# Kernel tuning notes

Hardware: AMD Instinct MI355X
Metric: run time of the kernel (lower is better)

Reference implementation:

```python
import jax, jax.numpy as jnp
import numpy as np

L, B, H, E, V = 64, 2048, 512, 50, 96
PAD = 0  # padding_idx of the char embedding


def setup_inputs() -> dict:
    key = jax.random.key(0)
    ks = jax.random.split(key, 10)
    s = 0.1  # param scale to keep gates in a sane range
    emb = jax.random.normal(ks[0], (V, E), jnp.float32) * s
    emb = emb.at[PAD].set(0.0)  # padding_idx row is zero
    return {
        "input_ids": jax.random.randint(ks[1], (L, B), 0, V),
        "h0": jax.random.normal(ks[2], (1, B, H), jnp.float32) * s,
        "c0": jax.random.normal(ks[3], (1, B, H), jnp.float32) * s,
        "emb": emb,
        "W_ih": jax.random.normal(ks[4], (4 * H, E), jnp.float32) * s,
        "W_hh": jax.random.normal(ks[5], (4 * H, H), jnp.float32) * s,
        "b_ih": jax.random.normal(ks[6], (4 * H,), jnp.float32) * s,
        "b_hh": jax.random.normal(ks[7], (4 * H,), jnp.float32) * s,
        "W_out": jax.random.normal(ks[8], (V, H), jnp.float32) * s,
        "b_out": jax.random.normal(ks[9], (V,), jnp.float32) * s,
    }


def reference(input_ids, h0, c0, emb, W_ih, W_hh, b_ih, b_hh, W_out, b_out):
    # Embedding lookup: (L, B, E)
    x = emb[input_ids]
    # Precompute input-side gate contributions for all steps: (L, B, 4H)
    x_gates = jnp.einsum('lbe,ge->lbg', x, W_ih) + b_ih + b_hh

    def step(carry, xg):
        h, c = carry  # (B, H) each
        gates = xg + h @ W_hh.T  # (B, 4H), PyTorch gate order i, f, g, o
        i, f, g, o = jnp.split(gates, 4, axis=-1)
        c_new = jax.nn.sigmoid(f) * c + jax.nn.sigmoid(i) * jnp.tanh(g)
        h_new = jax.nn.sigmoid(o) * jnp.tanh(c_new)
        return (h_new, c_new), h_new

    (hL, cL), hs = jax.lax.scan(step, (h0[0], c0[0]), x_gates)
    # Output projection on every step's hidden state: (L, B, V)
    scores = jnp.einsum('lbh,vh->lbv', hs, W_out) + b_out
    return scores, hL[None], cL[None]
```

## Files before the change

kernel.cpp:

```cpp
#include <hip/hip_runtime.h>
#include <stdint.h>

#define LSEQ 64
#define BATCH 2048
#define HID 512
#define NG 2048
#define KP 576
#define VOCAB 96
#define BH (BATCH*HID)

typedef unsigned short u16;
typedef __attribute__((ext_vector_type(8))) short short8;
typedef __attribute__((ext_vector_type(4))) float f32x4;

__device__ __forceinline__ u16 f2bf(float f) {
    union { float f; unsigned u; } v; v.f = f;
    return (u16)((v.u + 0x7FFFu + ((v.u >> 16) & 1u)) >> 16);
}
__device__ __forceinline__ float sig_(float x) { return 1.f / (1.f + __expf(-x)); }
__device__ __forceinline__ float th_(float x) {
    x = fminf(fmaxf(x, -30.f), 30.f);
    float e = __expf(2.f * x);
    return (e - 1.f) / (e + 1.f);
}
__device__ __forceinline__ void gld16(const void* g, void* l) {
    __builtin_amdgcn_global_load_lds(
        (const __attribute__((address_space(1))) unsigned int*)g,
        (__attribute__((address_space(3))) unsigned int*)l, 16, 0, 0);
}
__device__ __forceinline__ void gld16c(const void* g, void* l) {
    __builtin_amdgcn_global_load_lds(
        (const __attribute__((address_space(1))) unsigned int*)g,
        (__attribute__((address_space(3))) unsigned int*)l, 16, 0, 0x11);
}

__global__ void k_init(const float* __restrict__ h0, u16* __restrict__ hs0,
                       unsigned* __restrict__ flags) {
    int i = blockIdx.x * 256 + threadIdx.x;
    hs0[i] = f2bf(h0[i]);
    if (i < LSEQ * 256) flags[i] = 0;
}

__global__ void k_pack_w(const float* __restrict__ Wih, const float* __restrict__ Whh,
                         const float* __restrict__ bih, const float* __restrict__ bhh,
                         u16* __restrict__ Wp, float* __restrict__ bp) {
    int id = blockIdx.x * 256 + threadIdx.x;
    int n = id / 72, kc = id % 72;
    int j = n >> 2, q = n & 3;
    int src = q * HID + j;
    int k0 = kc * 8;
    unsigned pk[4];
#pragma unroll
    for (int t = 0; t < 4; ++t) {
        int k = k0 + 2 * t;
        float f0 = (k < 512) ? Whh[src * 512 + k] : ((k < 562) ? Wih[src * 50 + k - 512] : 0.f);
        float f1 = (k + 1 < 512) ? Whh[src * 512 + k + 1]
                                 : ((k + 1 < 562) ? Wih[src * 50 + k + 1 - 512] : 0.f);
        pk[t] = (unsigned)f2bf(f0) | ((unsigned)f2bf(f1) << 16);
    }
    *(uint4*)(Wp + (size_t)n * KP + k0) = make_uint4(pk[0], pk[1], pk[2], pk[3]);
    if (kc == 0) bp[n] = bih[src] + bhh[src];
}

__global__ void k_embed(const int* __restrict__ ids, const float* __restrict__ emb,
                        u16* __restrict__ xb) {
    int id = blockIdx.x * 256 + threadIdx.x;
    int row = id >> 3, kc = id & 7;
    int tok = ids[row];
    int k0 = kc * 8;
    unsigned pk[4];
#pragma unroll
    for (int t = 0; t < 4; ++t) {
        int k = k0 + 2 * t;
        unsigned lo = (k < 50) ? (unsigned)f2bf(emb[tok * 50 + k]) : 0u;
        unsigned hi = (k + 1 < 50) ? (unsigned)f2bf(emb[tok * 50 + k + 1]) : 0u;
        pk[t] = lo | (hi << 16);
    }
    *(uint4*)(xb + (size_t)row * 64 + k0) = make_uint4(pk[0], pk[1], pk[2], pk[3]);
}

__global__ void k_pack_wout(const float* __restrict__ Wo, u16* __restrict__ Wb) {
    int id = blockIdx.x * 256 + threadIdx.x;
    int k0 = id * 8;
    unsigned pk[4];
#pragma unroll
    for (int t = 0; t < 4; ++t)
        pk[t] = (unsigned)f2bf(Wo[k0 + 2 * t]) | ((unsigned)f2bf(Wo[k0 + 2 * t + 1]) << 16);
    *(uint4*)(Wb + k0) = make_uint4(pk[0], pk[1], pk[2], pk[3]);
}

__global__ __launch_bounds__(256, 1) void k_persist(
    const u16* __restrict__ xb, const u16* __restrict__ Wp,
    const float* __restrict__ bp, const float* __restrict__ c0,
    u16* __restrict__ hs, float* __restrict__ foutH, float* __restrict__ foutC,
    unsigned* __restrict__ flags)
{
    __shared__ char smem[65536];
    float* gsm = (float*)smem;

    const int tid = threadIdx.x;
    const int lane = tid & 63;
    const int w = tid >> 6;
    const int wm = w >> 1, wn = w & 1;
    const int bm = blockIdx.x & 15, bn = blockIdx.x >> 4;
    const int m0 = bm * 128, n0 = bn * 128;
    const int rsub = lane >> 3;
    const int colsw = (((lane & 7) ^ rsub) << 3);

    short8 bf[9][2][4];
#pragma unroll
    for (int kt = 0; kt < 9; ++kt)
#pragma unroll
        for (int kk = 0; kk < 2; ++kk)
#pragma unroll
            for (int j = 0; j < 4; ++j)
                bf[kt][kk][j] = *(const short8*)(
                    Wp + (size_t)(n0 + wn * 64 + j * 16 + (lane & 15)) * KP
                       + kt * 64 + kk * 32 + (lane >> 4) * 8);

    const int cp = tid & 15;
    const int rg = tid >> 4;
    const int swc = (rg & 7) << 2;
    float4 bb0 = *(const float4*)(bp + n0 + cp * 8);
    float4 bb1 = *(const float4*)(bp + n0 + cp * 8 + 4);
    float c[16];
#pragma unroll
    for (int rr = 0; rr < 8; ++rr)
#pragma unroll
        for (int cc = 0; cc < 2; ++cc)
            c[rr * 2 + cc] = c0[(size_t)(m0 + rg * 8 + rr) * HID + (n0 >> 2) + cp * 2 + cc];

#pragma unroll 1
    for (int l = 0; l < LSEQ; ++l) {
        const u16* hsrc = hs + (size_t)l * BH;

        {
            const u16* xs = xb + (size_t)l * BATCH * 64;
#pragma unroll
            for (int it = 0; it < 4; ++it) {
                int wc = w * 4 + it;
                gld16(xs + (size_t)(m0 + wc * 8 + rsub) * 64 + colsw, smem + wc * 1024);
            }
        }
        if (l > 0 && w == 0) {
            const unsigned* f = flags + (unsigned)(l - 1) * 256 + bm * 16;
            for (;;) {
                unsigned v = (lane < 16)
                    ? __hip_atomic_load(f + lane, __ATOMIC_RELAXED, __HIP_MEMORY_SCOPE_AGENT)
                    : 1u;
                if (__all(v != 0)) break;
                __builtin_amdgcn_s_sleep(2);
            }
        }
        __syncthreads();
        __builtin_amdgcn_sched_barrier(0);

#pragma unroll
        for (int it = 0; it < 4; ++it) {
            int wc = w * 4 + it;
            gld16c(hsrc + (size_t)(m0 + wc * 8 + rsub) * HID + colsw, smem + 16384 + wc * 1024);
        }

        f32x4 acc[4][4] = {};
#pragma unroll
        for (int i = 0; i < 9; ++i) {
            if (i > 0) {
                if (i < 8) asm volatile("s_waitcnt vmcnt(4)" ::: "memory");
                else       asm volatile("s_waitcnt vmcnt(0)" ::: "memory");
                __builtin_amdgcn_s_barrier();
                __builtin_amdgcn_sched_barrier(0);
            }
            if (i + 2 <= 8) {
                char* dst = smem + ((i + 2) % 3) * 16384;
#pragma unroll
                for (int it = 0; it < 4; ++it) {
                    int wc = w * 4 + it;
                    gld16c(hsrc + (size_t)(m0 + wc * 8 + rsub) * HID + (i + 1) * 64 + colsw,
                           dst + wc * 1024);
                }
            }
            const int kt = (i == 0) ? 8 : (i - 1);
            const u16* As_ = (const u16*)(smem + (i % 3) * 16384);
#pragma unroll
            for (int kk = 0; kk < 2; ++kk) {
                short8 av[4];
#pragma unroll
                for (int q = 0; q < 4; ++q)
                    av[q] = *(const short8*)(As_ + (wm * 64 + q * 16 + (lane & 15)) * 64
                                 + (((kk * 4 + (lane >> 4)) ^ (lane & 7)) << 3));
#pragma unroll
                for (int q = 0; q < 4; ++q)
#pragma unroll
                    for (int j = 0; j < 4; ++j)
                        acc[q][j] = __builtin_amdgcn_mfma_f32_16x16x32_bf16(
                            av[q], bf[kt][kk][j], acc[q][j], 0, 0, 0);
            }
        }
        __syncthreads();

#pragma unroll
        for (int q = 0; q < 4; ++q) {
            int ml = wm * 64 + q * 16 + ((lane >> 4) << 2);
#pragma unroll
            for (int j = 0; j < 4; ++j) {
                int nl = wn * 64 + j * 16 + (lane & 15);
#pragma unroll
                for (int r = 0; r < 4; ++r) {
                    int row = ml + r;
                    gsm[row * 128 + (nl ^ (((row >> 3) & 7) << 2))] = acc[q][j][r];
                }
            }
        }
        __syncthreads();

        u16* hdst = hs + (size_t)(l + 1) * BH;
        const bool last = (l == LSEQ - 1);
#pragma unroll
        for (int rr = 0; rr < 8; ++rr) {
            int row = rg * 8 + rr;
            const float* gp = gsm + row * 128;
            float4 g0 = *(const float4*)(gp + ((cp * 8) ^ swc));
            float4 g1 = *(const float4*)(gp + ((cp * 8 + 4) ^ swc));
            float gi0 = g0.x + bb0.x, gf0 = g0.y + bb0.y, gg0 = g0.z + bb0.z, go0 = g0.w + bb0.w;
            float gi1 = g1.x + bb1.x, gf1 = g1.y + bb1.y, gg1 = g1.z + bb1.z, go1 = g1.w + bb1.w;
            float cn0 = sig_(gf0) * c[rr * 2 + 0] + sig_(gi0) * th_(gg0);
            float cn1 = sig_(gf1) * c[rr * 2 + 1] + sig_(gi1) * th_(gg1);
            float hn0 = sig_(go0) * th_(cn0);
            float hn1 = sig_(go1) * th_(cn1);
            c[rr * 2 + 0] = cn0; c[rr * 2 + 1] = cn1;
            size_t ci = (size_t)(m0 + row) * HID + (n0 >> 2) + cp * 2;
            unsigned hp = (unsigned)f2bf(hn0) | ((unsigned)f2bf(hn1) << 16);
            __hip_atomic_store((unsigned*)(hdst + ci), hp,
                               __ATOMIC_RELAXED, __HIP_MEMORY_SCOPE_AGENT);
            if (last) { foutH[ci] = hn0; foutH[ci + 1] = hn1;
                        foutC[ci] = cn0; foutC[ci + 1] = cn1; }
        }
        asm volatile("s_waitcnt vmcnt(0)" ::: "memory");
        __syncthreads();
        if (tid == 0)
            __hip_atomic_store(flags + (unsigned)l * 256 + bm * 16 + bn, 1u,
                               __ATOMIC_RELAXED, __HIP_MEMORY_SCOPE_AGENT);
    }
}

__global__ __launch_bounds__(256) void k_scores(
    const u16* __restrict__ hsall, const u16* __restrict__ Wb,
    const float* __restrict__ bo, float* __restrict__ out)
{
    __shared__ char smem[28672];
    u16* As = (u16*)smem;
    u16* Bs = (u16*)(smem + 16384);
    const int tid = threadIdx.x, lane = tid & 63, w = tid >> 6;
    const size_t m0 = (size_t)blockIdx.x * 128;
    const int colo = (lane & 7) * 8;
    const int rsub = lane >> 3;
    f32x4 acc[2][6] = {};

    for (int kt = 0; kt < 8; ++kt) {
#pragma unroll
        for (int it = 0; it < 4; ++it) {
            int wc = w * 4 + it;
            int r = wc * 8 + rsub;
            gld16(hsall + (m0 + r) * 512 + kt * 64 + colo, smem + wc * 1024);
        }
#pragma unroll
        for (int it = 0; it < 3; ++it) {
            int wc = w * 3 + it;
            int r = wc * 8 + rsub;
            gld16(Wb + (size_t)r * 512 + kt * 64 + colo, smem + 16384 + wc * 1024);
        }
        __syncthreads();
#pragma unroll
        for (int kk = 0; kk < 2; ++kk) {
            short8 av[2], bv[6];
#pragma unroll
            for (int i = 0; i < 2; ++i)
                av[i] = *(const short8*)(As + (w * 32 + i * 16 + (lane & 15)) * 64 + kk * 32 + (lane >> 4) * 8);
#pragma unroll
            for (int j = 0; j < 6; ++j)
                bv[j] = *(const short8*)(Bs + (j * 16 + (lane & 15)) * 64 + kk * 32 + (lane >> 4) * 8);
#pragma unroll
            for (int i = 0; i < 2; ++i)
#pragma unroll
                for (int j = 0; j < 6; ++j)
                    acc[i][j] = __builtin_amdgcn_mfma_f32_16x16x32_bf16(av[i], bv[j], acc[i][j], 0, 0, 0);
        }
        __syncthreads();
    }
#pragma unroll
    for (int i = 0; i < 2; ++i) {
        int ml = w * 32 + i * 16 + (lane >> 4) * 4;
#pragma unroll
        for (int j = 0; j < 6; ++j) {
            int v = j * 16 + (lane & 15);
            float bb = bo[v];
#pragma unroll
            for (int r = 0; r < 4; ++r)
                out[(m0 + ml + r) * 96 + v] = acc[i][j][r] + bb;
        }
    }
}

extern "C" void kernel_launch(void* const* d_in, const int* in_sizes, int n_in,
                              void* d_out, int out_size, void* d_ws, size_t ws_size,
                              hipStream_t stream) {
    const int*   ids  = (const int*)d_in[0];
    const float* h0   = (const float*)d_in[1];
    const float* c0   = (const float*)d_in[2];
    const float* emb  = (const float*)d_in[3];
    const float* Wih  = (const float*)d_in[4];
    const float* Whh  = (const float*)d_in[5];
    const float* bih  = (const float*)d_in[6];
    const float* bhh  = (const float*)d_in[7];
    const float* Wout = (const float*)d_in[8];
    const float* bout = (const float*)d_in[9];

    char* ws = (char*)d_ws;
    u16*      hs    = (u16*)ws;
    unsigned* flags = (unsigned*)(ws + 136314880);
    u16*      xb    = (u16*)(ws + 140509184);
    u16*      Wp    = (u16*)(ws + 157286400);
    float*    bp    = (float*)(ws + 159645696);
    u16*      Wb    = (u16*)(ws + 159653888);
    float*    out   = (float*)d_out;

    k_init<<<dim3(BH / 256), dim3(256), 0, stream>>>(h0, hs, flags);
    k_pack_w<<<dim3(NG * 72 / 256), dim3(256), 0, stream>>>(Wih, Whh, bih, bhh, Wp, bp);
    k_embed<<<dim3(LSEQ * BATCH * 8 / 256), dim3(256), 0, stream>>>(ids, emb, xb);
    k_pack_wout<<<dim3(VOCAB * HID / 8 / 256), dim3(256), 0, stream>>>(Wout, Wb);

    k_persist<<<dim3(256), dim3(256), 0, stream>>>(
        xb, Wp, bp, c0, hs, out + 12582912, out + 12582912 + BH, flags);

    k_scores<<<dim3(LSEQ * BATCH / 128), dim3(256), 0, stream>>>(hs + BH, Wb, bout, out);
}
```

Before: 644.9 us.

## Issue all hidden-state K-tile loads upfront into nine LDS buffers per step

Replaces the 3-stage rotating LDS ring for the recurrent h tiles with 144KB of dynamic shared memory holding all nine 16KB K-tiles. All 32 global-to-LDS loads are issued at once after the flag wait, and each MFMA K-step waits on a decreasing vmcnt, which removes the per-iteration barrier-then-issue dependency and exposes more memory parallelism on the latency-critical recurrent step. It also drops the cache-policy bits (0x11) on the h loads, so they now use default caching, and replaces __syncthreads with a raw s_barrier. The large LDS footprint relies on the MI355X's larger LDS and keeps occupancy at one block per CU.

```diff
diff --git a/kernel.cpp b/kernel.cpp
--- a/kernel.cpp
+++ b/kernel.cpp
@@ -28,11 +28,7 @@
         (const __attribute__((address_space(1))) unsigned int*)g,
         (__attribute__((address_space(3))) unsigned int*)l, 16, 0, 0);
 }
-__device__ __forceinline__ void gld16c(const void* g, void* l) {
-    __builtin_amdgcn_global_load_lds(
-        (const __attribute__((address_space(1))) unsigned int*)g,
-        (__attribute__((address_space(3))) unsigned int*)l, 16, 0, 0x11);
-}
+#define WAITV(n) asm volatile("s_waitcnt vmcnt(" #n ")" ::: "memory")
 
 __global__ void k_init(const float* __restrict__ h0, u16* __restrict__ hs0,
                        unsigned* __restrict__ flags) {
@@ -95,7 +91,7 @@
     u16* __restrict__ hs, float* __restrict__ foutH, float* __restrict__ foutC,
     unsigned* __restrict__ flags)
 {
-    __shared__ char smem[65536];
+    extern __shared__ char smem[];
     float* gsm = (float*)smem;
 
     const int tid = threadIdx.x;
@@ -152,35 +148,34 @@
                 __builtin_amdgcn_s_sleep(2);
             }
         }
-        __syncthreads();
+        __builtin_amdgcn_s_barrier();
         __builtin_amdgcn_sched_barrier(0);
 
 #pragma unroll
-        for (int it = 0; it < 4; ++it) {
-            int wc = w * 4 + it;
-            gld16c(hsrc + (size_t)(m0 + wc * 8 + rsub) * HID + colsw, smem + 16384 + wc * 1024);
+        for (int t = 0; t < 8; ++t) {
+            char* dst = smem + (t + 1) * 16384;
+#pragma unroll
+            for (int it = 0; it < 4; ++it) {
+                int wc = w * 4 + it;
+                gld16(hsrc + (size_t)(m0 + wc * 8 + rsub) * HID + t * 64 + colsw,
+                      dst + wc * 1024);
+            }
         }
 
         f32x4 acc[4][4] = {};
 #pragma unroll
-        for (int i = 0; i < 9; ++i) {
-            if (i > 0) {
-                if (i < 8) asm volatile("s_waitcnt vmcnt(4)" ::: "memory");
-                else       asm volatile("s_waitcnt vmcnt(0)" ::: "memory");
-                __builtin_amdgcn_s_barrier();
-                __builtin_amdgcn_sched_barrier(0);
-            }
-            if (i + 2 <= 8) {
-                char* dst = smem + ((i + 2) % 3) * 16384;
-#pragma unroll
-                for (int it = 0; it < 4; ++it) {
-                    int wc = w * 4 + it;
-                    gld16c(hsrc + (size_t)(m0 + wc * 8 + rsub) * HID + (i + 1) * 64 + colsw,
-                           dst + wc * 1024);
-                }
-            }
-            const int kt = (i == 0) ? 8 : (i - 1);
-            const u16* As_ = (const u16*)(smem + (i % 3) * 16384);
+        for (int t = 0; t < 9; ++t) {
+            switch (t) {
+                case 0: WAITV(32); break; case 1: WAITV(28); break;
+                case 2: WAITV(24); break; case 3: WAITV(20); break;
+                case 4: WAITV(16); break; case 5: WAITV(12); break;
+                case 6: WAITV(8);  break; case 7: WAITV(4);  break;
+                default: WAITV(0); break;
+            }
+            __builtin_amdgcn_s_barrier();
+            __builtin_amdgcn_sched_barrier(0);
+            const int kt = (t == 0) ? 8 : (t - 1);
+            const u16* As_ = (const u16*)(smem + t * 16384);
 #pragma unroll
             for (int kk = 0; kk < 2; ++kk) {
                 short8 av[4];
@@ -235,7 +230,7 @@
             if (last) { foutH[ci] = hn0; foutH[ci + 1] = hn1;
                         foutC[ci] = cn0; foutC[ci + 1] = cn1; }
         }
-        asm volatile("s_waitcnt vmcnt(0)" ::: "memory");
+        WAITV(0);
         __syncthreads();
         if (tid == 0)
             __hip_atomic_store(flags + (unsigned)l * 256 + bm * 16 + bn, 1u,
@@ -329,7 +324,9 @@
     k_embed<<<dim3(LSEQ * BATCH * 8 / 256), dim3(256), 0, stream>>>(ids, emb, xb);
     k_pack_wout<<<dim3(VOCAB * HID / 8 / 256), dim3(256), 0, stream>>>(Wout, Wb);
 
-    k_persist<<<dim3(256), dim3(256), 0, stream>>>(
+    hipFuncSetAttribute((const void*)k_persist,
+                        hipFuncAttributeMaxDynamicSharedMemorySize, 147456);
+    k_persist<<<dim3(256), dim3(256), 147456, stream>>>(
         xb, Wp, bp, c0, hs, out + 12582912, out + 12582912 + BH, flags);
 
     k_scores<<<dim3(LSEQ * BATCH / 128), dim3(256), 0, stream>>>(hs + BH, Wb, bout, out);
```

Result: slower. 696.4 us (+8.0%).

## Swap MFMA operands in persistent LSTM and fuse gate epilogue in registers

Applied to the files above, without the earlier changes.

The recurrent GEMM is rearranged so weights form the A operand and hidden state the B operand. Each lane's accumulator then holds all four gates (i,f,g,o) of one unit, so the cell update runs straight from registers and the fp32 LDS round trip with its extra barrier is gone. Weights are split: three k-tiles stay in registers and six are staged once into a large dynamic LDS area (about 152 KB). The new h is packed through a small swizzled LDS buffer and written with coalesced 16-byte stores instead of per-element atomics, and cache-policy bits on the h loads are dropped, which risks stale reads across workgroups.

```diff
diff --git a/kernel.cpp b/kernel.cpp
--- a/kernel.cpp
+++ b/kernel.cpp
@@ -9,6 +9,11 @@
 #define VOCAB 96
 #define BH (BATCH*HID)
 
+#define WLDS_OFF 0
+#define RING_OFF 98304
+#define HPK_OFF  147456
+#define SMEM_TOT 155648
+
 typedef unsigned short u16;
 typedef __attribute__((ext_vector_type(8))) short short8;
 typedef __attribute__((ext_vector_type(4))) float f32x4;
@@ -28,11 +33,7 @@
         (const __attribute__((address_space(1))) unsigned int*)g,
         (__attribute__((address_space(3))) unsigned int*)l, 16, 0, 0);
 }
-__device__ __forceinline__ void gld16c(const void* g, void* l) {
-    __builtin_amdgcn_global_load_lds(
-        (const __attribute__((address_space(1))) unsigned int*)g,
-        (__attribute__((address_space(3))) unsigned int*)l, 16, 0, 0x11);
-}
+#define WAITV(n) asm volatile("s_waitcnt vmcnt(" #n ")" ::: "memory")
 
 __global__ void k_init(const float* __restrict__ h0, u16* __restrict__ hs0,
                        unsigned* __restrict__ flags) {
@@ -95,8 +96,10 @@
     u16* __restrict__ hs, float* __restrict__ foutH, float* __restrict__ foutC,
     unsigned* __restrict__ flags)
 {
-    __shared__ char smem[65536];
-    float* gsm = (float*)smem;
+    extern __shared__ char smem[];
+    char* Wlds = smem + WLDS_OFF;
+    char* ring = smem + RING_OFF;
+    u16*  hpk  = (u16*)(smem + HPK_OFF);
 
     const int tid = threadIdx.x;
     const int lane = tid & 63;
@@ -106,29 +109,45 @@
     const int m0 = bm * 128, n0 = bn * 128;
     const int rsub = lane >> 3;
     const int colsw = (((lane & 7) ^ rsub) << 3);
-
-    short8 bf[9][2][4];
-#pragma unroll
-    for (int kt = 0; kt < 9; ++kt)
+    const int bsub = lane & 15;
+    const int usub = lane >> 4;
+
+#pragma unroll
+    for (int t = 0; t < 6; ++t)
+#pragma unroll
+        for (int it = 0; it < 4; ++it) {
+            int wc = w * 4 + it;
+            gld16(Wp + (size_t)(n0 + wc * 8 + rsub) * KP + (t + 2) * 64 + colsw,
+                  Wlds + t * 16384 + wc * 1024);
+        }
+
+    short8 wreg[3][2][4];
+#pragma unroll
+    for (int t = 0; t < 3; ++t) {
+        const int koff = (t == 0) ? 512 : (t - 1) * 64;
 #pragma unroll
         for (int kk = 0; kk < 2; ++kk)
 #pragma unroll
-            for (int j = 0; j < 4; ++j)
-                bf[kt][kk][j] = *(const short8*)(
-                    Wp + (size_t)(n0 + wn * 64 + j * 16 + (lane & 15)) * KP
-                       + kt * 64 + kk * 32 + (lane >> 4) * 8);
-
-    const int cp = tid & 15;
-    const int rg = tid >> 4;
-    const int swc = (rg & 7) << 2;
-    float4 bb0 = *(const float4*)(bp + n0 + cp * 8);
-    float4 bb1 = *(const float4*)(bp + n0 + cp * 8 + 4);
-    float c[16];
-#pragma unroll
-    for (int rr = 0; rr < 8; ++rr)
-#pragma unroll
-        for (int cc = 0; cc < 2; ++cc)
-            c[rr * 2 + cc] = c0[(size_t)(m0 + rg * 8 + rr) * HID + (n0 >> 2) + cp * 2 + cc];
+            for (int qm = 0; qm < 4; ++qm)
+                wreg[t][kk][qm] = *(const short8*)(
+                    Wp + (size_t)(n0 + wm * 64 + qm * 16 + bsub) * KP
+                       + koff + kk * 32 + usub * 8);
+    }
+
+    float4 bb[4];
+#pragma unroll
+    for (int qm = 0; qm < 4; ++qm)
+        bb[qm] = *(const float4*)(bp + n0 + wm * 64 + qm * 16 + usub * 4);
+    float c[4][4];
+#pragma unroll
+    for (int qm = 0; qm < 4; ++qm)
+#pragma unroll
+        for (int qn = 0; qn < 4; ++qn)
+            c[qm][qn] = c0[(size_t)(m0 + wn * 64 + qn * 16 + bsub) * HID
+                           + (n0 >> 2) + wm * 16 + qm * 4 + usub];
+
+    WAITV(0);
+    __syncthreads();
 
 #pragma unroll 1
     for (int l = 0; l < LSEQ; ++l) {
@@ -139,7 +158,7 @@
 #pragma unroll
             for (int it = 0; it < 4; ++it) {
                 int wc = w * 4 + it;
-                gld16(xs + (size_t)(m0 + wc * 8 + rsub) * 64 + colsw, smem + wc * 1024);
+                gld16(xs + (size_t)(m0 + wc * 8 + rsub) * 64 + colsw, ring + wc * 1024);
             }
         }
         if (l > 0 && w == 0) {
@@ -158,84 +177,96 @@
 #pragma unroll
         for (int it = 0; it < 4; ++it) {
             int wc = w * 4 + it;
-            gld16c(hsrc + (size_t)(m0 + wc * 8 + rsub) * HID + colsw, smem + 16384 + wc * 1024);
+            gld16(hsrc + (size_t)(m0 + wc * 8 + rsub) * HID + colsw,
+                  ring + 16384 + wc * 1024);
         }
 
         f32x4 acc[4][4] = {};
 #pragma unroll
         for (int i = 0; i < 9; ++i) {
             if (i > 0) {
-                if (i < 8) asm volatile("s_waitcnt vmcnt(4)" ::: "memory");
-                else       asm volatile("s_waitcnt vmcnt(0)" ::: "memory");
+                if (i < 8) WAITV(4); else WAITV(0);
                 __builtin_amdgcn_s_barrier();
                 __builtin_amdgcn_sched_barrier(0);
             }
             if (i + 2 <= 8) {
-                char* dst = smem + ((i + 2) % 3) * 16384;
+                char* dst = ring + ((i + 2) % 3) * 16384;
 #pragma unroll
                 for (int it = 0; it < 4; ++it) {
                     int wc = w * 4 + it;
-                    gld16c(hsrc + (size_t)(m0 + wc * 8 + rsub) * HID + (i + 1) * 64 + colsw,
-                           dst + wc * 1024);
+                    gld16(hsrc + (size_t)(m0 + wc * 8 + rsub) * HID + (i + 1) * 64 + colsw,
+                          dst + wc * 1024);
                 }
             }
-            const int kt = (i == 0) ? 8 : (i - 1);
-            const u16* As_ = (const u16*)(smem + (i % 3) * 16384);
+            const u16* Bs_ = (const u16*)(ring + (i % 3) * 16384);
 #pragma unroll
             for (int kk = 0; kk < 2; ++kk) {
-                short8 av[4];
-#pragma unroll
-                for (int q = 0; q < 4; ++q)
-                    av[q] = *(const short8*)(As_ + (wm * 64 + q * 16 + (lane & 15)) * 64
-                                 + (((kk * 4 + (lane >> 4)) ^ (lane & 7)) << 3));
-#pragma unroll
-                for (int q = 0; q < 4; ++q)
-#pragma unroll
-                    for (int j = 0; j < 4; ++j)
-                        acc[q][j] = __builtin_amdgcn_mfma_f32_16x16x32_bf16(
-                            av[q], bf[kt][kk][j], acc[q][j], 0, 0, 0);
-            }
-        }
-        __syncthreads();
-
-#pragma unroll
-        for (int q = 0; q < 4; ++q) {
-            int ml = wm * 64 + q * 16 + ((lane >> 4) << 2);
-#pragma unroll
-            for (int j = 0; j < 4; ++j) {
-                int nl = wn * 64 + j * 16 + (lane & 15);
-#pragma unroll
-                for (int r = 0; r < 4; ++r) {
-                    int row = ml + r;
-                    gsm[row * 128 + (nl ^ (((row >> 3) & 7) << 2))] = acc[q][j][r];
+                short8 hv[4];
+#pragma unroll
+                for (int qn = 0; qn < 4; ++qn)
+                    hv[qn] = *(const short8*)(Bs_ + (wn * 64 + qn * 16 + bsub) * 64
+                                 + (((kk * 4 + usub) ^ (lane & 7)) << 3));
+                short8 wf[4];
+                if (i <= 2) {
+#pragma unroll
+                    for (int qm = 0; qm < 4; ++qm) wf[qm] = wreg[i][kk][qm];
+                } else {
+                    const u16* Ws_ = (const u16*)(Wlds + (i - 3) * 16384);
+#pragma unroll
+                    for (int qm = 0; qm < 4; ++qm)
+                        wf[qm] = *(const short8*)(Ws_ + (wm * 64 + qm * 16 + bsub) * 64
+                                     + (((kk * 4 + usub) ^ (lane & 7)) << 3));
                 }
-            }
-        }
-        __syncthreads();
-
-        u16* hdst = hs + (size_t)(l + 1) * BH;
+#pragma unroll
+                for (int qm = 0; qm < 4; ++qm)
+#pragma unroll
+                    for (int qn = 0; qn < 4; ++qn)
+                        acc[qm][qn] = __builtin_amdgcn_mfma_f32_16x16x32_bf16(
+                            wf[qm], hv[qn], acc[qm][qn], 0, 0, 0);
+            }
+        }
+
         const bool last = (l == LSEQ - 1);
 #pragma unroll
-        for (int rr = 0; rr < 8; ++rr) {
-            int row = rg * 8 + rr;
-            const float* gp = gsm + row * 128;
-            float4 g0 = *(const float4*)(gp + ((cp * 8) ^ swc));
-            float4 g1 = *(const float4*)(gp + ((cp * 8 + 4) ^ swc));
-            float gi0 = g0.x + bb0.x, gf0 = g0.y + bb0.y, gg0 = g0.z + bb0.z, go0 = g0.w + bb0.w;
-            float gi1 = g1.x + bb1.x, gf1 = g1.y + bb1.y, gg1 = g1.z + bb1.z, go1 = g1.w + bb1.w;
-            float cn0 = sig_(gf0) * c[rr * 2 + 0] + sig_(gi0) * th_(gg0);
-            float cn1 = sig_(gf1) * c[rr * 2 + 1] + sig_(gi1) * th_(gg1);
-            float hn0 = sig_(go0) * th_(cn0);
-            float hn1 = sig_(go1) * th_(cn1);
-            c[rr * 2 + 0] = cn0; c[rr * 2 + 1] = cn1;
-            size_t ci = (size_t)(m0 + row) * HID + (n0 >> 2) + cp * 2;
-            unsigned hp = (unsigned)f2bf(hn0) | ((unsigned)f2bf(hn1) << 16);
-            __hip_atomic_store((unsigned*)(hdst + ci), hp,
-                               __ATOMIC_RELAXED, __HIP_MEMORY_SCOPE_AGENT);
-            if (last) { foutH[ci] = hn0; foutH[ci + 1] = hn1;
-                        foutC[ci] = cn0; foutC[ci + 1] = cn1; }
-        }
-        asm volatile("s_waitcnt vmcnt(0)" ::: "memory");
+        for (int qm = 0; qm < 4; ++qm) {
+            const float4 b4 = bb[qm];
+            const int u_loc = wm * 16 + qm * 4 + usub;
+#pragma unroll
+            for (int qn = 0; qn < 4; ++qn) {
+                const int b_loc = wn * 64 + qn * 16 + bsub;
+                float gi = acc[qm][qn][0] + b4.x;
+                float gf = acc[qm][qn][1] + b4.y;
+                float gg = acc[qm][qn][2] + b4.z;
+                float go = acc[qm][qn][3] + b4.w;
+                float cn = sig_(gf) * c[qm][qn] + sig_(gi) * th_(gg);
+                float hn = sig_(go) * th_(cn);
+                c[qm][qn] = cn;
+                hpk[b_loc * 32 + (u_loc ^ ((b_loc & 7) << 2))] = f2bf(hn);
+                if (last) {
+                    size_t ci = (size_t)(m0 + b_loc) * HID + (n0 >> 2) + u_loc;
+                    foutH[ci] = hn; foutC[ci] = cn;
+                }
+            }
+        }
+        __syncthreads();
+
+        {
+            const int b = tid >> 1, hf = tid & 1;
+            unsigned long long q[4];
+#pragma unroll
+            for (int g = 0; g < 4; ++g) {
+                int G = hf * 4 + g;
+                int gs = G ^ (b & 7);
+                q[g] = *(const unsigned long long*)((const char*)hpk + b * 64 + gs * 8);
+            }
+            u16* dst = hs + (size_t)(l + 1) * BH + (size_t)(m0 + b) * HID
+                       + (n0 >> 2) + hf * 16;
+            *(uint4*)(dst)     = make_uint4((unsigned)q[0], (unsigned)(q[0] >> 32),
+                                            (unsigned)q[1], (unsigned)(q[1] >> 32));
+            *(uint4*)(dst + 8) = make_uint4((unsigned)q[2], (unsigned)(q[2] >> 32),
+                                            (unsigned)q[3], (unsigned)(q[3] >> 32));
+        }
+        WAITV(0);
         __syncthreads();
         if (tid == 0)
             __hip_atomic_store(flags + (unsigned)l * 256 + bm * 16 + bn, 1u,
@@ -293,10 +324,10 @@
 #pragma unroll
         for (int j = 0; j < 6; ++j) {
             int v = j * 16 + (lane & 15);
-            float bb = bo[v];
+            float bbv = bo[v];
 #pragma unroll
             for (int r = 0; r < 4; ++r)
-                out[(m0 + ml + r) * 96 + v] = acc[i][j][r] + bb;
+                out[(m0 + ml + r) * 96 + v] = acc[i][j][r] + bbv;
         }
     }
 }
@@ -329,7 +360,9 @@
     k_embed<<<dim3(LSEQ * BATCH * 8 / 256), dim3(256), 0, stream>>>(ids, emb, xb);
     k_pack_wout<<<dim3(VOCAB * HID / 8 / 256), dim3(256), 0, stream>>>(Wout, Wb);
 
-    k_persist<<<dim3(256), dim3(256), 0, stream>>>(
+    hipFuncSetAttribute((const void*)k_persist,
+                        hipFuncAttributeMaxDynamicSharedMemorySize, SMEM_TOT);
+    k_persist<<<dim3(256), dim3(256), SMEM_TOT, stream>>>(
         xb, Wp, bp, c0, hs, out + 12582912, out + 12582912 + BH, flags);
 
     k_scores<<<dim3(LSEQ * BATCH / 128), dim3(256), 0, stream>>>(hs + BH, Wb, bout, out);
```

After: 577.2 us. -10.5%, faster.
